# Kernel tuning notes

Hardware: AMD Instinct MI355X
Metric: run time of the kernel (lower is better)

Reference implementation:

```python
import jax, jax.numpy as jnp
import numpy as np
import math

NUM_HEADS = 16
NUM_KV_HEADS = 4
HEAD_DIM = 128


def rotate_half(x):
    x1, x2 = x[..., : x.shape[-1] // 2], x[..., x.shape[-1] // 2 :]
    return jnp.concatenate((-x2, x1), axis=-1)


def setup_inputs() -> dict:
    key = jax.random.key(0)
    ks = jax.random.split(key, 7)
    B, L, D = 2, 2048, 2048
    hidden_states = jax.random.normal(ks[0], (B, L, D), dtype=jnp.float32)
    # realistic RoPE tables
    inv_freq = 1.0 / (10000.0 ** (np.arange(0, HEAD_DIM, 2, dtype=np.float32) / HEAD_DIM))
    t = np.arange(L, dtype=np.float32)
    freqs = np.outer(t, inv_freq)
    emb = np.concatenate([freqs, freqs], axis=-1)
    cos = jnp.asarray(np.cos(emb), dtype=jnp.float32)
    sin = jnp.asarray(np.sin(emb), dtype=jnp.float32)
    s = 1.0 / math.sqrt(D)
    Wq = jax.random.normal(ks[1], (D, NUM_HEADS * HEAD_DIM), dtype=jnp.float32) * s
    Wk = jax.random.normal(ks[2], (D, NUM_KV_HEADS * HEAD_DIM), dtype=jnp.float32) * s
    Wv = jax.random.normal(ks[3], (D, NUM_KV_HEADS * HEAD_DIM), dtype=jnp.float32) * s
    Wo = jax.random.normal(ks[4], (NUM_HEADS * HEAD_DIM, D), dtype=jnp.float32) * s
    return {"hidden_states": hidden_states, "cos": cos, "sin": sin,
            "Wq": Wq, "Wk": Wk, "Wv": Wv, "Wo": Wo}


def reference(hidden_states, cos, sin, Wq, Wk, Wv, Wo):
    B, L, D = hidden_states.shape
    H, KVH, Dh = NUM_HEADS, NUM_KV_HEADS, HEAD_DIM
    q = (hidden_states @ Wq).reshape(B, L, H, Dh)
    k = (hidden_states @ Wk).reshape(B, L, KVH, Dh)
    v = (hidden_states @ Wv).reshape(B, L, KVH, Dh)
    # RoPE: cos/sin are [L, Dh] broadcast over batch and heads
    c = cos[None, :, None, :]
    s = sin[None, :, None, :]
    q = q * c + rotate_half(q) * s
    k = k * c + rotate_half(k) * s
    # GQA: repeat kv heads to match query heads
    rep = H // KVH
    k = jnp.repeat(k, rep, axis=2)
    v = jnp.repeat(v, rep, axis=2)
    scale = 1.0 / math.sqrt(Dh)
    # [B, H, L, L]
    attn = jnp.einsum('bqhd,bkhd->bhqk', q, k) * scale
    i = jnp.arange(L)[:, None]
    j = jnp.arange(L)[None, :]
    attn = jnp.where(i >= j, attn, -jnp.inf)
    attn = jax.nn.softmax(attn, axis=-1)
    out = jnp.einsum('bhqk,bkhd->bqhd', attn, v).reshape(B, L, H * Dh)
    return out @ Wo
```

## Files before the change

### kernel.cpp

```cpp
#include <hip/hip_runtime.h>
#include <hip/hip_bf16.h>

typedef __attribute__((ext_vector_type(8))) short bf16x8;
typedef __attribute__((ext_vector_type(4))) float f32x4;
typedef __attribute__((ext_vector_type(4))) short short4v;

__device__ __forceinline__ unsigned short f2bf(float f) {
  union { float f; unsigned u; } x; x.f = f;
  return (unsigned short)((x.u + 0x7FFFu + ((x.u >> 16) & 1u)) >> 16);
}

__device__ __forceinline__ short f2bf_hw(float f) {
  __hip_bfloat16 h = __float2bfloat16(f);
  return *(short*)&h;
}

__device__ __forceinline__ void lds_cp16(const void* g, void* l) {
  __builtin_amdgcn_global_load_lds(
      (const __attribute__((address_space(1))) void*)g,
      (__attribute__((address_space(3))) void*)l,
      16, 0, 0);
}

#define GBAR() do { __builtin_amdgcn_s_barrier(); __builtin_amdgcn_sched_barrier(0); } while (0)

__global__ __launch_bounds__(256) void cast_x(const float* __restrict__ in,
                                              short* __restrict__ out, int n4) {
  int i = blockIdx.x * 256 + threadIdx.x;
  if (i >= n4) return;
  float4 v = reinterpret_cast<const float4*>(in)[i];
  short4v o;
  o.x = (short)f2bf(v.x); o.y = (short)f2bf(v.y);
  o.z = (short)f2bf(v.z); o.w = (short)f2bf(v.w);
  reinterpret_cast<short4v*>(out)[i] = o;
}

__global__ __launch_bounds__(256) void transp_cast(const float* __restrict__ in,
                                                   short* __restrict__ out,
                                                   int K, int N) {
  __shared__ float t[32][33];
  int bn = blockIdx.x * 32, bk = blockIdx.y * 32;
  int tx = threadIdx.x, ty = threadIdx.y;
  for (int i = ty; i < 32; i += 8)
    t[i][tx] = in[(size_t)(bk + i) * N + bn + tx];
  __syncthreads();
  for (int i = ty; i < 32; i += 8)
    out[(size_t)(bn + i) * K + bk + tx] = (short)f2bf(t[tx][i]);
}

__global__ __launch_bounds__(256) void transp_qkv(const float* __restrict__ Wq,
                                                  const float* __restrict__ Wk,
                                                  const float* __restrict__ Wv,
                                                  short* __restrict__ out) {
  __shared__ float t[32][33];
  const int K = 2048;
  int bnG = blockIdx.x * 32;
  int bk = blockIdx.y * 32;
  const float* src; int N, bn;
  if (bnG < 2048)      { src = Wq; N = 2048; bn = bnG; }
  else if (bnG < 2560) { src = Wk; N = 512;  bn = bnG - 2048; }
  else                 { src = Wv; N = 512;  bn = bnG - 2560; }
  int tx = threadIdx.x, ty = threadIdx.y;
  for (int i = ty; i < 32; i += 8)
    t[i][tx] = src[(size_t)(bk + i) * N + bn + tx];
  __syncthreads();
  for (int i = ty; i < 32; i += 8)
    out[(size_t)(bnG + i) * K + bk + tx] = (short)f2bf(t[tx][i]);
}

__global__ __launch_bounds__(256) void transp_v(const short* __restrict__ V,
                                                short* __restrict__ VTo) {
  __shared__ short t[32][34];
  const int hd = blockIdx.z;
  const int p0 = blockIdx.x * 32, d0 = blockIdx.y * 32;
  const short* src = V + (size_t)hd * 2048 * 128;
  short* dst = VTo + (size_t)hd * 2048 * 128;
  int tx = threadIdx.x, ty = threadIdx.y;
  for (int i = ty; i < 32; i += 8)
    t[i][tx] = src[(size_t)(p0 + i) * 128 + d0 + tx];
  __syncthreads();
  for (int i = ty; i < 32; i += 8)
    dst[(size_t)(d0 + i) * 2048 + p0 + tx] = t[tx][i];
}

template <int BM, int EPI>
__global__ __launch_bounds__(512, 2) void gemm8p(
    const short* __restrict__ A, const short* __restrict__ Bt,
    float* __restrict__ C,
    short* __restrict__ Qo, short* __restrict__ Ko, short* __restrict__ Vo,
    const float* __restrict__ cosT, const float* __restrict__ sinT,
    int N, int Kd, int nbm) {
  constexpr int NM = BM / 64;
  __shared__ __align__(16) short As[2][BM * 64];
  __shared__ __align__(16) short Bs[2][256 * 64];
  const int tid = threadIdx.x;
  const int l = tid & 63, l15 = l & 15, l4 = l >> 4;
  const int wid = tid >> 6, wr = wid >> 1, wc = wid & 1;
  const int cpx = gridDim.x >> 3;
  const int sid = (blockIdx.x & 7) * cpx + (blockIdx.x >> 3);
  const int bm = sid % nbm, bn = sid / nbm;

  const int srow = tid >> 3;
  const int sch = tid & 7;

  auto stA = [&](int dbuf, int k0, int i) {
    const int rl = srow + i * 64;
    const int c = sch ^ (rl & 7);
    lds_cp16(A + (size_t)(bm * BM + rl) * Kd + k0 + c * 8,
             (char*)As[dbuf] + tid * 16 + i * 8192);
  };
  auto stB = [&](int dbuf, int k0, int j) {
    const int rl = srow + j * 64;
    const int c = sch ^ (rl & 7);
    lds_cp16(Bt + (size_t)(bn * 256 + rl) * Kd + k0 + c * 8,
             (char*)Bs[dbuf] + tid * 16 + j * 8192);
  };
  auto rdA = [&](int dbuf, int m, int kb) {
    const int row = wr * (BM / 4) + m * 16 + l15;
    return *(const bf16x8*)((const char*)As[dbuf] + (row << 7) +
                            ((kb * 64 + l4 * 16) ^ ((row & 7) << 4)));
  };
  auto rdB = [&](int dbuf, int nh, int f, int kb) {
    const int row = wc * 128 + nh * 64 + f * 16 + l15;
    return *(const bf16x8*)((const char*)Bs[dbuf] + (row << 7) +
                            ((kb * 64 + l4 * 16) ^ ((row & 7) << 4)));
  };

  f32x4 acc[NM][8];
#pragma unroll
  for (int m = 0; m < NM; m++)
#pragma unroll
    for (int n = 0; n < 8; n++) acc[m][n] = (f32x4){0.f, 0.f, 0.f, 0.f};

  const int NT = Kd >> 6;

#pragma unroll
  for (int i = 0; i < NM; i++) stA(0, 0, i);
#pragma unroll
  for (int j = 0; j < 4; j++) stB(0, 0, j);
  asm volatile("s_waitcnt vmcnt(0)" ::: "memory");
  GBAR();

  for (int kt = 0; kt < NT; kt++) {
    const int buf = kt & 1, nbf = buf ^ 1;
    const bool stg = (kt + 1 < NT);
    const int k1 = (kt + 1) << 6;
    bf16x8 a[NM], b[4];

#pragma unroll
    for (int m = 0; m < NM; m++) a[m] = rdA(buf, m, 0);
#pragma unroll
    for (int f = 0; f < 4; f++) b[f] = rdB(buf, 0, f, 0);
    if (stg) { stA(nbf, k1, 0); stA(nbf, k1, 1); }
    if (stg) asm volatile("s_waitcnt vmcnt(2)" ::: "memory");
    else     asm volatile("s_waitcnt vmcnt(0)" ::: "memory");
    GBAR();
    asm volatile("s_waitcnt lgkmcnt(0)" ::: "memory");
    __builtin_amdgcn_sched_barrier(0);
    __builtin_amdgcn_s_setprio(1);
#pragma unroll
    for (int m = 0; m < NM; m++)
#pragma unroll
      for (int f = 0; f < 4; f++)
        acc[m][f] = __builtin_amdgcn_mfma_f32_16x16x32_bf16(a[m], b[f], acc[m][f], 0, 0, 0);
    __builtin_amdgcn_s_setprio(0);
    GBAR();

#pragma unroll
    for (int f = 0; f < 4; f++) b[f] = rdB(buf, 1, f, 0);
    if (stg) {
      if (BM == 256) { stA(nbf, k1, 2); stA(nbf, k1, 3); }
      else           { stB(nbf, k1, 0); stB(nbf, k1, 2); }
    }
    GBAR();
    asm volatile("s_waitcnt lgkmcnt(0)" ::: "memory");
    __builtin_amdgcn_sched_barrier(0);
    __builtin_amdgcn_s_setprio(1);
#pragma unroll
    for (int m = 0; m < NM; m++)
#pragma unroll
      for (int f = 0; f < 4; f++)
        acc[m][4 + f] = __builtin_amdgcn_mfma_f32_16x16x32_bf16(a[m], b[f], acc[m][4 + f], 0, 0, 0);
    __builtin_amdgcn_s_setprio(0);
    GBAR();

#pragma unroll
    for (int m = 0; m < NM; m++) a[m] = rdA(buf, m, 1);
#pragma unroll
    for (int f = 0; f < 4; f++) b[f] = rdB(buf, 0, f, 1);
    if (stg) {
      if (BM == 256) { stB(nbf, k1, 0); stB(nbf, k1, 2); }
      else           { stB(nbf, k1, 1); stB(nbf, k1, 3); }
    }
    GBAR();
    asm volatile("s_waitcnt lgkmcnt(0)" ::: "memory");
    __builtin_amdgcn_sched_barrier(0);
    __builtin_amdgcn_s_setprio(1);
#pragma unroll
    for (int m = 0; m < NM; m++)
#pragma unroll
      for (int f = 0; f < 4; f++)
        acc[m][f] = __builtin_amdgcn_mfma_f32_16x16x32_bf16(a[m], b[f], acc[m][f], 0, 0, 0);
    __builtin_amdgcn_s_setprio(0);
    GBAR();

#pragma unroll
    for (int f = 0; f < 4; f++) b[f] = rdB(buf, 1, f, 1);
    if (stg && BM == 256) { stB(nbf, k1, 1); stB(nbf, k1, 3); }
    if (stg) asm volatile("s_waitcnt vmcnt(2)" ::: "memory");
    GBAR();
    asm volatile("s_waitcnt lgkmcnt(0)" ::: "memory");
    __builtin_amdgcn_sched_barrier(0);
    __builtin_amdgcn_s_setprio(1);
#pragma unroll
    for (int m = 0; m < NM; m++)
#pragma unroll
      for (int f = 0; f < 4; f++)
        acc[m][4 + f] = __builtin_amdgcn_mfma_f32_16x16x32_bf16(a[m], b[f], acc[m][4 + f], 0, 0, 0);
    __builtin_amdgcn_s_setprio(0);
    GBAR();
  }

  if (EPI == 0) {
#pragma unroll
    for (int m = 0; m < NM; m++) {
      const int grow = bm * BM + wr * (BM / 4) + m * 16 + l4 * 4;
#pragma unroll
      for (int ni = 0; ni < 8; ni++) {
        const int col = bn * 256 + wc * 128 + (ni >> 2) * 64 + (ni & 3) * 16 + l15;
#pragma unroll
        for (int r = 0; r < 4; r++)
          C[(size_t)(grow + r) * N + col] = acc[m][ni][r];
      }
    }
  } else {
    const int head = bn * 2 + wc;
#pragma unroll
    for (int m = 0; m < NM; m++) {
#pragma unroll
      for (int r = 0; r < 4; r++) {
        const int grow = bm * BM + wr * (BM / 4) + m * 16 + l4 * 4 + r;
        const int bb = grow >> 11, pos = grow & 2047;
        if (head < 20) {
          float c4[4], s4[4];
#pragma unroll
          for (int ni = 0; ni < 4; ni++) {
            const int dh = ni * 16 + l15;
            c4[ni] = cosT[pos * 128 + dh];
            s4[ni] = sinT[pos * 128 + dh];
          }
          short* dst;
          if (head < 16) dst = Qo + ((size_t)(bb * 16 + head) * 2048 + pos) * 128;
          else           dst = Ko + ((size_t)(bb * 4 + (head - 16)) * 2048 + pos) * 128;
#pragma unroll
          for (int ni = 0; ni < 4; ni++) {
            const int dh = ni * 16 + l15;
            float xlo = acc[m][ni][r], xhi = acc[m][ni + 4][r];
            dst[dh]      = (short)f2bf(xlo * c4[ni] - xhi * s4[ni]);
            dst[dh + 64] = (short)f2bf(xhi * c4[ni] + xlo * s4[ni]);
          }
        } else {
          short* dst = Vo + ((size_t)(bb * 4 + (head - 20)) * 2048 + pos) * 128;
#pragma unroll
          for (int ni = 0; ni < 8; ni++)
            dst[(ni >> 2) * 64 + (ni & 3) * 16 + l15] = (short)f2bf(acc[m][ni][r]);
        }
      }
    }
  }
}

__global__ __launch_bounds__(256) void attn_fwd(
    const short* __restrict__ Q, const short* __restrict__ K,
    const short* __restrict__ VT, short* __restrict__ AO) {
  __shared__ __align__(16) short Ks[2][64 * 128];
  __shared__ __align__(16) short VTs[2][128 * 64];
  __shared__ __align__(16) short Pl[4][16 * 64];
  const int tid = threadIdx.x;
  const int w = tid >> 6, l = tid & 63;
  const int l15 = l & 15, l4 = l >> 4;
  const int bid = blockIdx.x;
  const int lg = (bid & 7) * 64 + (bid >> 3);
  const int bh = lg >> 4, pp = lg & 15;
  const int b = bh >> 4, h = bh & 15, kv = h >> 2;
  const short* Qbase = Q + (size_t)(b * 16 + h) * 2048 * 128;
  const short* Kbase = K + (size_t)(b * 4 + kv) * 2048 * 128;
  const short* VTb   = VT + (size_t)(b * 4 + kv) * 2048 * 128;

  int rk[4], ck[4], dv[4], kc[4];
#pragma unroll
  for (int i = 0; i < 4; i++) {
    const int c = tid + i * 256;
    rk[i] = c >> 4; ck[i] = (c & 15) ^ (rk[i] & 7);
    dv[i] = c >> 3; kc[i] = (c & 7) ^ (dv[i] & 7);
  }

  const float SCL = 0.08838834764831845f * 1.4426950408889634f;

  bf16x8 ones;
#pragma unroll
  for (int j = 0; j < 8; j++) ones[j] = (short)0x3F80;

  for (int qq = 0; qq < 2; qq++) {
    const int qt = qq ? (31 - pp) : pp;
    const int q0w = qt * 64 + w * 16;

    bf16x8 qf[4];
#pragma unroll
    for (int kb = 0; kb < 4; kb++)
      qf[kb] = *(const bf16x8*)(Qbase + (size_t)(q0w + l15) * 128 + kb * 32 + l4 * 8);

    f32x4 oacc[8];
#pragma unroll
    for (int i = 0; i < 8; i++) oacc[i] = (f32x4){0.f, 0.f, 0.f, 0.f};
    f32x4 lacc = (f32x4){0.f, 0.f, 0.f, 0.f};

    const int ntiles = qt + 1;

    __syncthreads();
#pragma unroll
    for (int i = 0; i < 4; i++) {
      lds_cp16(Kbase + rk[i] * 128 + ck[i] * 8, (char*)Ks[0] + i * 4096 + tid * 16);
      lds_cp16(VTb + (size_t)dv[i] * 2048 + kc[i] * 8, (char*)VTs[0] + i * 4096 + tid * 16);
    }

    for (int nt = 0; nt < ntiles; nt++) {
      const int k0 = nt * 64, buf = nt & 1;
      __syncthreads();
      if (nt + 1 < ntiles) {
        const int kn = k0 + 64, bnx = buf ^ 1;
#pragma unroll
        for (int i = 0; i < 4; i++) {
          lds_cp16(Kbase + (size_t)(kn + rk[i]) * 128 + ck[i] * 8,
                   (char*)Ks[bnx] + i * 4096 + tid * 16);
          lds_cp16(VTb + (size_t)dv[i] * 2048 + kn + kc[i] * 8,
                   (char*)VTs[bnx] + i * 4096 + tid * 16);
        }
      }

      f32x4 sa[4];
#pragma unroll
      for (int kg = 0; kg < 4; kg++) sa[kg] = (f32x4){0.f, 0.f, 0.f, 0.f};
      __builtin_amdgcn_s_setprio(1);
#pragma unroll
      for (int kg = 0; kg < 4; kg++) {
        const int row = kg * 16 + l15;
        const int swz = (row & 7) << 4;
#pragma unroll
        for (int kb = 0; kb < 4; kb++) {
          const char* kp = (const char*)Ks[buf] + row * 256 + ((kb * 64 + l4 * 16) ^ swz);
          sa[kg] = __builtin_amdgcn_mfma_f32_16x16x32_bf16(qf[kb], *(const bf16x8*)kp, sa[kg], 0, 0, 0);
        }
      }
      __builtin_amdgcn_s_setprio(0);

      float p[4][4];
      const bool domask = (k0 + 63 > q0w);
#pragma unroll
      for (int kg = 0; kg < 4; kg++)
#pragma unroll
        for (int r = 0; r < 4; r++) {
          float pv = exp2f(sa[kg][r] * SCL);
          if (domask) {
            int qrow = q0w + l4 * 4 + r;
            if (k0 + kg * 16 + l15 > qrow) pv = 0.f;
          }
          p[kg][r] = pv;
        }

#pragma unroll
      for (int r = 0; r < 4; r++) {
        const int rw = l4 * 4 + r;
        const int swz = (rw & 7) << 4;
#pragma unroll
        for (int kg = 0; kg < 4; kg++)
          *(short*)((char*)Pl[w] + (rw * 128 + ((kg * 32 + l15 * 2) ^ swz))) =
              f2bf_hw(p[kg][r]);
      }
      asm volatile("s_waitcnt lgkmcnt(0)" ::: "memory");
      bf16x8 pf[2];
#pragma unroll
      for (int ks = 0; ks < 2; ks++)
        pf[ks] = *(const bf16x8*)((const char*)Pl[w] +
                 (l15 * 128 + ((ks * 64 + l4 * 16) ^ ((l15 & 7) << 4))));

      __builtin_amdgcn_s_setprio(1);
#pragma unroll
      for (int nb = 0; nb < 8; nb++) {
        const int d = nb * 16 + l15;
        const int dsw = (d & 7) << 4;
#pragma unroll
        for (int ks = 0; ks < 2; ks++) {
          const char* vp = (const char*)VTs[buf] + d * 128 + ((ks * 64 + l4 * 16) ^ dsw);
          oacc[nb] = __builtin_amdgcn_mfma_f32_16x16x32_bf16(pf[ks], *(const bf16x8*)vp, oacc[nb], 0, 0, 0);
        }
      }
      lacc = __builtin_amdgcn_mfma_f32_16x16x32_bf16(pf[0], ones, lacc, 0, 0, 0);
      lacc = __builtin_amdgcn_mfma_f32_16x16x32_bf16(pf[1], ones, lacc, 0, 0, 0);
      __builtin_amdgcn_s_setprio(0);
    }

#pragma unroll
    for (int r = 0; r < 4; r++) {
      float inv = 1.0f / lacc[r];
      size_t rowb = ((size_t)b * 2048 + q0w + l4 * 4 + r) * 2048 + h * 128;
#pragma unroll
      for (int nb = 0; nb < 8; nb++)
        AO[rowb + nb * 16 + l15] = f2bf_hw(oacc[nb][r] * inv);
    }
  }
}

extern "C" void kernel_launch(void* const* d_in, const int* in_sizes, int n_in,
                              void* d_out, int out_size, void* d_ws, size_t ws_size,
                              hipStream_t stream) {
  const float* hs   = (const float*)d_in[0];
  const float* cosT = (const float*)d_in[1];
  const float* sinT = (const float*)d_in[2];
  const float* Wq   = (const float*)d_in[3];
  const float* Wk   = (const float*)d_in[4];
  const float* Wv   = (const float*)d_in[5];
  const float* Wo   = (const float*)d_in[6];
  float* out = (float*)d_out;

  char* p = (char*)d_ws;
  short* Xb   = (short*)p; p += (size_t)4096 * 2048 * 2;
  short* Wqkv = (short*)p; p += (size_t)3072 * 2048 * 2;
  short* Wot  = (short*)p; p += (size_t)2048 * 2048 * 2;
  short* Qb   = (short*)p; p += (size_t)2 * 16 * 2048 * 128 * 2;
  short* Kb   = (short*)p; p += (size_t)2 * 4 * 2048 * 128 * 2;
  short* Vb   = (short*)p; p += (size_t)2 * 4 * 2048 * 128 * 2;
  short* VTb  = (short*)p; p += (size_t)2 * 4 * 2048 * 128 * 2;
  short* AO   = Xb;

  cast_x<<<8192, 256, 0, stream>>>(hs, Xb, 2097152);
  transp_qkv<<<dim3(96, 64), dim3(32, 8), 0, stream>>>(Wq, Wk, Wv, Wqkv);
  transp_cast<<<dim3(64, 64), dim3(32, 8), 0, stream>>>(Wo, Wot, 2048, 2048);

  gemm8p<256, 1><<<192, 512, 0, stream>>>(Xb, Wqkv, nullptr, Qb, Kb, Vb,
                                          cosT, sinT, 3072, 2048, 16);
  transp_v<<<dim3(64, 4, 8), dim3(32, 8), 0, stream>>>(Vb, VTb);
  attn_fwd<<<512, 256, 0, stream>>>(Qb, Kb, VTb, AO);
  gemm8p<128, 0><<<256, 512, 0, stream>>>(AO, Wot, out, nullptr, nullptr, nullptr,
                                          nullptr, nullptr, 2048, 2048, 32);
}
```

Measured before the change: 217.2 us.

## Add dedicated QKV GEMM kernel with finer-grained 8-phase staging and wave layout

Replaces the templated 256x256 QKV GEMM with a dedicated kernel. It splits the A and B tiles into 128-row halves, uses a 2x4 wave layout, and runs an 8-phase schedule per pair of K-steps, with each phase issuing one half-tile prefetch. The RoPE epilogue is reorganised so each lane handles one dh column and reads cos/sin once per row. The aim is better overlap of global-to-LDS loads with MFMA and fewer LDS reads per MFMA. The cost is more barriers per iteration and a more complex prefetch ordering, which is sensitive to vmcnt correctness.

```diff
diff --git a/kernel.cpp b/kernel.cpp
--- a/kernel.cpp
+++ b/kernel.cpp
@@ -83,13 +83,129 @@
     dst[(size_t)(d0 + i) * 2048 + p0 + tx] = t[tx][i];
 }
 
-template <int BM, int EPI>
+__global__ __launch_bounds__(512, 2) void qkv8p(
+    const short* __restrict__ A, const short* __restrict__ Bt,
+    short* __restrict__ Qo, short* __restrict__ Ko, short* __restrict__ Vo,
+    const float* __restrict__ cosT, const float* __restrict__ sinT) {
+  __shared__ __align__(16) short As[2][2][8192];
+  __shared__ __align__(16) short Bs[2][2][8192];
+  const int tid = threadIdx.x;
+  const int l = tid & 63, l15 = l & 15, l4 = l >> 4;
+  const int wid = tid >> 6, wr = wid >> 2, wc = wid & 3;
+  const int sid = (blockIdx.x & 7) * 24 + (blockIdx.x >> 3);
+  const int bm = sid & 15, bn = sid >> 4;
+  const int swz = (l15 & 7) << 4;
+
+  const int c0r = tid >> 3, c0s = (tid & 7) ^ (c0r & 7);
+  const int c1r = (tid + 512) >> 3, c1s = (tid & 7) ^ (c1r & 7);
+
+  auto SA = [&](int t, int h) {
+    if (t >= 32) return;
+    short* dst = As[t & 1][h];
+    lds_cp16(A + (size_t)(bm * 256 + h * 128 + c0r) * 2048 + t * 64 + c0s * 8,
+             (char*)dst + tid * 16);
+    lds_cp16(A + (size_t)(bm * 256 + h * 128 + c1r) * 2048 + t * 64 + c1s * 8,
+             (char*)dst + tid * 16 + 8192);
+  };
+  auto SB = [&](int t, int h) {
+    if (t >= 32) return;
+    short* dst = Bs[t & 1][h];
+    lds_cp16(Bt + (size_t)(bn * 256 + h * 128 + c0r) * 2048 + t * 64 + c0s * 8,
+             (char*)dst + tid * 16);
+    lds_cp16(Bt + (size_t)(bn * 256 + h * 128 + c1r) * 2048 + t * 64 + c1s * 8,
+             (char*)dst + tid * 16 + 8192);
+  };
+  auto rdA = [&](int d, int mh, int ml, int ks) {
+    const int lr = wr * 16 + ml * 32 + l15;
+    return *(const bf16x8*)((const char*)As[d][mh] + lr * 128 + ((ks * 64 + l4 * 16) ^ swz));
+  };
+  auto rdB = [&](int d, int nh, int nl, int ks) {
+    const int lc = wc * 16 + nl * 64 + l15;
+    return *(const bf16x8*)((const char*)Bs[d][nh] + lc * 128 + ((ks * 64 + l4 * 16) ^ swz));
+  };
+
+  f32x4 acc[8][4];
+#pragma unroll
+  for (int m = 0; m < 8; m++)
+#pragma unroll
+    for (int n = 0; n < 4; n++) acc[m][n] = (f32x4){0.f, 0.f, 0.f, 0.f};
+
+  SA(0, 0); SB(0, 0); SB(0, 1); SA(0, 1); SA(1, 0); SB(1, 0);
+  asm volatile("s_waitcnt vmcnt(8)" ::: "memory");
+  GBAR();
+
+  for (int I = 0; I < 16; I++) {
+    const int T = 2 * I;
+    auto phase = [&](int d, int mh, int nh, auto stage) {
+      bf16x8 a[4][2], b[2][2];
+#pragma unroll
+      for (int ml = 0; ml < 4; ml++)
+#pragma unroll
+        for (int ks = 0; ks < 2; ks++) a[ml][ks] = rdA(d, mh, ml, ks);
+#pragma unroll
+      for (int nl = 0; nl < 2; nl++)
+#pragma unroll
+        for (int ks = 0; ks < 2; ks++) b[nl][ks] = rdB(d, nh, nl, ks);
+      stage();
+      asm volatile("s_waitcnt vmcnt(8)" ::: "memory");
+      GBAR();
+      asm volatile("s_waitcnt lgkmcnt(0)" ::: "memory");
+      __builtin_amdgcn_sched_barrier(0);
+      __builtin_amdgcn_s_setprio(1);
+#pragma unroll
+      for (int ml = 0; ml < 4; ml++)
+#pragma unroll
+        for (int nl = 0; nl < 2; nl++)
+#pragma unroll
+          for (int ks = 0; ks < 2; ks++)
+            acc[mh * 4 + ml][nh * 2 + nl] = __builtin_amdgcn_mfma_f32_16x16x32_bf16(
+                a[ml][ks], b[nl][ks], acc[mh * 4 + ml][nh * 2 + nl], 0, 0, 0);
+      __builtin_amdgcn_s_setprio(0);
+      GBAR();
+    };
+    phase(0, 0, 0, [&] { SB(T + 1, 1); });
+    phase(0, 0, 1, [&] { SA(T + 1, 1); });
+    phase(0, 1, 0, [&] { SA(T + 2, 0); });
+    phase(0, 1, 1, [&] { SB(T + 2, 0); });
+    phase(1, 0, 0, [&] { SB(T + 2, 1); });
+    phase(1, 0, 1, [&] { SA(T + 2, 1); });
+    phase(1, 1, 0, [&] { SA(T + 3, 0); });
+    phase(1, 1, 1, [&] { SB(T + 3, 0); });
+  }
+
+#pragma unroll
+  for (int m = 0; m < 8; m++) {
+#pragma unroll
+    for (int ri = 0; ri < 4; ri++) {
+      const int grow = bm * 256 + (wr + 2 * m) * 16 + l4 * 4 + ri;
+      const int bb = grow >> 11, pos = grow & 2047;
+      const int dh = wc * 16 + l15;
+      const float cv = cosT[pos * 128 + dh];
+      const float sv = sinT[pos * 128 + dh];
+#pragma unroll
+      for (int hp = 0; hp < 2; hp++) {
+        const int head = bn * 2 + hp;
+        const float xlo = acc[m][2 * hp][ri], xhi = acc[m][2 * hp + 1][ri];
+        short* dst;
+        if (head < 16)      dst = Qo + ((size_t)(bb * 16 + head) * 2048 + pos) * 128;
+        else if (head < 20) dst = Ko + ((size_t)(bb * 4 + head - 16) * 2048 + pos) * 128;
+        else                dst = Vo + ((size_t)(bb * 4 + head - 20) * 2048 + pos) * 128;
+        if (head < 20) {
+          dst[dh]      = (short)f2bf(xlo * cv - xhi * sv);
+          dst[dh + 64] = (short)f2bf(xhi * cv + xlo * sv);
+        } else {
+          dst[dh]      = (short)f2bf(xlo);
+          dst[dh + 64] = (short)f2bf(xhi);
+        }
+      }
+    }
+  }
+}
+
+template <int BM>
 __global__ __launch_bounds__(512, 2) void gemm8p(
     const short* __restrict__ A, const short* __restrict__ Bt,
-    float* __restrict__ C,
-    short* __restrict__ Qo, short* __restrict__ Ko, short* __restrict__ Vo,
-    const float* __restrict__ cosT, const float* __restrict__ sinT,
-    int N, int Kd, int nbm) {
+    float* __restrict__ C, int N, int Kd, int nbm) {
   constexpr int NM = BM / 64;
   __shared__ __align__(16) short As[2][BM * 64];
   __shared__ __align__(16) short Bs[2][256 * 64];
@@ -168,10 +284,7 @@
 
 #pragma unroll
     for (int f = 0; f < 4; f++) b[f] = rdB(buf, 1, f, 0);
-    if (stg) {
-      if (BM == 256) { stA(nbf, k1, 2); stA(nbf, k1, 3); }
-      else           { stB(nbf, k1, 0); stB(nbf, k1, 2); }
-    }
+    if (stg) { stB(nbf, k1, 0); stB(nbf, k1, 2); }
     GBAR();
     asm volatile("s_waitcnt lgkmcnt(0)" ::: "memory");
     __builtin_amdgcn_sched_barrier(0);
@@ -188,10 +301,7 @@
     for (int m = 0; m < NM; m++) a[m] = rdA(buf, m, 1);
 #pragma unroll
     for (int f = 0; f < 4; f++) b[f] = rdB(buf, 0, f, 1);
-    if (stg) {
-      if (BM == 256) { stB(nbf, k1, 0); stB(nbf, k1, 2); }
-      else           { stB(nbf, k1, 1); stB(nbf, k1, 3); }
-    }
+    if (stg) { stB(nbf, k1, 1); stB(nbf, k1, 3); }
     GBAR();
     asm volatile("s_waitcnt lgkmcnt(0)" ::: "memory");
     __builtin_amdgcn_sched_barrier(0);
@@ -206,7 +316,6 @@
 
 #pragma unroll
     for (int f = 0; f < 4; f++) b[f] = rdB(buf, 1, f, 1);
-    if (stg && BM == 256) { stB(nbf, k1, 1); stB(nbf, k1, 3); }
     if (stg) asm volatile("s_waitcnt vmcnt(2)" ::: "memory");
     GBAR();
     asm volatile("s_waitcnt lgkmcnt(0)" ::: "memory");
@@ -221,51 +330,15 @@
     GBAR();
   }
 
-  if (EPI == 0) {
-#pragma unroll
-    for (int m = 0; m < NM; m++) {
-      const int grow = bm * BM + wr * (BM / 4) + m * 16 + l4 * 4;
-#pragma unroll
-      for (int ni = 0; ni < 8; ni++) {
-        const int col = bn * 256 + wc * 128 + (ni >> 2) * 64 + (ni & 3) * 16 + l15;
-#pragma unroll
-        for (int r = 0; r < 4; r++)
-          C[(size_t)(grow + r) * N + col] = acc[m][ni][r];
-      }
-    }
-  } else {
-    const int head = bn * 2 + wc;
-#pragma unroll
-    for (int m = 0; m < NM; m++) {
-#pragma unroll
-      for (int r = 0; r < 4; r++) {
-        const int grow = bm * BM + wr * (BM / 4) + m * 16 + l4 * 4 + r;
-        const int bb = grow >> 11, pos = grow & 2047;
-        if (head < 20) {
-          float c4[4], s4[4];
-#pragma unroll
-          for (int ni = 0; ni < 4; ni++) {
-            const int dh = ni * 16 + l15;
-            c4[ni] = cosT[pos * 128 + dh];
-            s4[ni] = sinT[pos * 128 + dh];
-          }
-          short* dst;
-          if (head < 16) dst = Qo + ((size_t)(bb * 16 + head) * 2048 + pos) * 128;
-          else           dst = Ko + ((size_t)(bb * 4 + (head - 16)) * 2048 + pos) * 128;
-#pragma unroll
-          for (int ni = 0; ni < 4; ni++) {
-            const int dh = ni * 16 + l15;
-            float xlo = acc[m][ni][r], xhi = acc[m][ni + 4][r];
-            dst[dh]      = (short)f2bf(xlo * c4[ni] - xhi * s4[ni]);
-            dst[dh + 64] = (short)f2bf(xhi * c4[ni] + xlo * s4[ni]);
-          }
-        } else {
-          short* dst = Vo + ((size_t)(bb * 4 + (head - 20)) * 2048 + pos) * 128;
-#pragma unroll
-          for (int ni = 0; ni < 8; ni++)
-            dst[(ni >> 2) * 64 + (ni & 3) * 16 + l15] = (short)f2bf(acc[m][ni][r]);
-        }
-      }
+#pragma unroll
+  for (int m = 0; m < NM; m++) {
+    const int grow = bm * BM + wr * (BM / 4) + m * 16 + l4 * 4;
+#pragma unroll
+    for (int ni = 0; ni < 8; ni++) {
+      const int col = bn * 256 + wc * 128 + (ni >> 2) * 64 + (ni & 3) * 16 + l15;
+#pragma unroll
+      for (int r = 0; r < 4; r++)
+        C[(size_t)(grow + r) * N + col] = acc[m][ni][r];
     }
   }
 }
@@ -437,10 +510,8 @@
   transp_qkv<<<dim3(96, 64), dim3(32, 8), 0, stream>>>(Wq, Wk, Wv, Wqkv);
   transp_cast<<<dim3(64, 64), dim3(32, 8), 0, stream>>>(Wo, Wot, 2048, 2048);
 
-  gemm8p<256, 1><<<192, 512, 0, stream>>>(Xb, Wqkv, nullptr, Qb, Kb, Vb,
-                                          cosT, sinT, 3072, 2048, 16);
+  qkv8p<<<192, 512, 0, stream>>>(Xb, Wqkv, Qb, Kb, Vb, cosT, sinT);
   transp_v<<<dim3(64, 4, 8), dim3(32, 8), 0, stream>>>(Vb, VTb);
   attn_fwd<<<512, 256, 0, stream>>>(Qb, Kb, VTb, AO);
-  gemm8p<128, 0><<<256, 512, 0, stream>>>(AO, Wot, out, nullptr, nullptr, nullptr,
-                                          nullptr, nullptr, 2048, 2048, 32);
-}
+  gemm8p<128><<<256, 512, 0, stream>>>(AO, Wot, out, 2048, 2048, 32);
+}
```

Measured after the change: 237.8 us. 1.09x slower.
